# Performance work log

Hardware: AMD Instinct MI355X
Metric: run time of the kernel (lower is better)

The kernel has to match this reference:

```python
import jax, jax.numpy as jnp
import numpy as np

B, S, D, H, NATT = 8, 512, 768, 256, 11  # batch, seq, d_model, gru hidden, n attention branches


def setup_inputs() -> dict:
    key = jax.random.key(0)
    ks = jax.random.split(key, 20)
    w = lambda k, shp, s=0.02: (jax.random.normal(k, shp, jnp.float32) * s)
    emb = w(ks[0], (7, D), 1.0).at[0].set(0.0)  # padding_idx=0 row is zero
    return {
        "essay_amlabel": jax.random.randint(ks[1], (B, S), 0, 7),
        "sequence_output": jax.random.normal(ks[2], (B, S, D), jnp.float32),
        "emb_table": emb,
        "Wq": w(ks[3], (NATT, D, D)), "bq": jnp.zeros((NATT, D), jnp.float32),
        "Wk": w(ks[4], (NATT, D, D)), "bk": jnp.zeros((NATT, D), jnp.float32),
        "Wv": w(ks[5], (NATT, D, D)), "bv": jnp.zeros((NATT, D), jnp.float32),
        "gru_Wih": w(ks[6], (2, 3 * H, D), 1.0 / np.sqrt(H)),
        "gru_Whh": w(ks[7], (2, 3 * H, H), 1.0 / np.sqrt(H)),
        "gru_bih": jnp.zeros((2, 3 * H), jnp.float32),
        "gru_bhh": jnp.zeros((2, 3 * H), jnp.float32),
        "W1": w(ks[8], (2 * H, 1)), "b1": jnp.zeros((1,), jnp.float32),
    }


def _gru_final_hidden(x, Wih, Whh, bih, bhh, reverse):
    # x: [N, S, D] -> final hidden [N, H] (PyTorch GRU equations)
    xp = jnp.einsum('nsd,hd->snh', x, Wih) + bih  # [S, N, 3H]

    def step(h, xt):
        gh = h @ Whh.T + bhh
        i_r, i_z, i_n = jnp.split(xt, 3, axis=-1)
        h_r, h_z, h_n = jnp.split(gh, 3, axis=-1)
        r = jax.nn.sigmoid(i_r + h_r)
        z = jax.nn.sigmoid(i_z + h_z)
        n = jnp.tanh(i_n + r * h_n)
        h_new = (1.0 - z) * n + z * h
        return h_new, None

    h0 = jnp.zeros((x.shape[0], Whh.shape[1]), x.dtype)
    h_final, _ = jax.lax.scan(step, h0, xp, reverse=reverse)
    return h_final


def reference(essay_amlabel, sequence_output, emb_table, Wq, bq, Wk, bk, Wv, bv,
              gru_Wih, gru_Whh, gru_bih, gru_bhh, W1, b1):
    am = emb_table[essay_amlabel]  # [B, S, D] queries
    # 11 independent attentions, num_heads=1, dropout=0 (eval) -> stack on axis k
    Q = jax.nn.relu(jnp.einsum('bsd,kde->kbse', am, Wq) + bq[:, None, None, :])
    K = jax.nn.relu(jnp.einsum('bsd,kde->kbse', sequence_output, Wk) + bk[:, None, None, :])
    V = jax.nn.relu(jnp.einsum('bsd,kde->kbse', sequence_output, Wv) + bv[:, None, None, :])
    scores = jnp.einsum('kbqd,kbmd->kbqm', Q, K) / jnp.sqrt(jnp.float32(D))
    attn = jax.nn.softmax(scores, axis=-1)
    qmask = jnp.sign(jnp.abs(jnp.sum(am, axis=-1)))  # [B, S]
    attn = attn * qmask[None, :, :, None]  # post-softmax query mask (as in source)
    out = jnp.einsum('kbqm,kbmd->kbqd', attn, V) + am[None]  # residual with queries
    eloutput = out + sequence_output[None]  # [11, B, S, D]
    gru_in = eloutput.reshape(NATT * B, S, D)
    h_f = _gru_final_hidden(gru_in, gru_Wih[0], gru_Whh[0], gru_bih[0], gru_bhh[0], False)
    h_b = _gru_final_hidden(gru_in, gru_Wih[1], gru_Whh[1], gru_bih[1], gru_bhh[1], True)
    final = jnp.concatenate([h_f, h_b], axis=-1)  # [11B, 2H]
    reshaped = final.reshape(NATT, B, 2 * H).transpose(1, 0, 2)  # [B, 11, 2H]
    logits = jax.nn.sigmoid(reshaped @ W1 + b1).squeeze(-1)  # [B, 11]
    return logits
```

## Files before the change

### kernel.cpp

```cpp
#include <hip/hip_runtime.h>
#include <hip/hip_bf16.h>
#include <hip/hip_fp16.h>
#include <math.h>

typedef __hip_bfloat16 bf16;
typedef __attribute__((ext_vector_type(8))) short short8;
typedef __attribute__((ext_vector_type(4))) float f32x4;

#define NATT 11
#define Bb 8
#define Ss 512
#define Dd 768
#define Hh 256
#define WSLICE 589824L

__device__ __forceinline__ void stf(float* p, float v) { *p = v; }
__device__ __forceinline__ void stf(bf16* p, float v) { *p = __float2bfloat16(v); }

__device__ __forceinline__ float blo(unsigned u) { return __uint_as_float(u << 16); }
__device__ __forceinline__ float bhi(unsigned u) { return __uint_as_float(u & 0xffff0000u); }
__device__ __forceinline__ float b2f(unsigned short u) { return __uint_as_float(((unsigned)u) << 16); }

__device__ __forceinline__ float ldg_any(const void* base, long idx, int flag) {
  if (flag) return ((const float*)base)[idx];
  return __bfloat162float(((const bf16*)base)[idx]);
}

__device__ __forceinline__ unsigned packh2(float a, float b) {
  __half2 hh = __floats2half2_rn(a, b);
  return __builtin_bit_cast(unsigned, hh);
}
__device__ __forceinline__ unsigned short f2h(float v) {
  __half h = __float2half(v);
  return __builtin_bit_cast(unsigned short, h);
}

typedef _Float16 f16x2 __attribute__((ext_vector_type(2)));

__device__ __forceinline__ float dot2u(unsigned a, unsigned b, float c) {
#if __has_builtin(__builtin_amdgcn_fdot2)
  return __builtin_amdgcn_fdot2(__builtin_bit_cast(f16x2, a),
                                __builtin_bit_cast(f16x2, b), c, false);
#else
  __half2 ah = __builtin_bit_cast(__half2, a);
  __half2 bh = __builtin_bit_cast(__half2, b);
  float2 af = __half22float2(ah), bf = __half22float2(bh);
  return c + af.x * bf.x + af.y * bf.y;
#endif
}

__device__ __forceinline__ float quad_sum(float v) {
#if __has_builtin(__builtin_amdgcn_update_dpp)
  int y = __builtin_amdgcn_update_dpp(0, __builtin_bit_cast(int, v), 0xB1, 0xF, 0xF, true);
  v += __builtin_bit_cast(float, y);
  y = __builtin_amdgcn_update_dpp(0, __builtin_bit_cast(int, v), 0x4E, 0xF, 0xF, true);
  v += __builtin_bit_cast(float, y);
  return v;
#else
  v += __shfl_xor(v, 1);
  v += __shfl_xor(v, 2);
  return v;
#endif
}

__device__ __forceinline__ void lds_barrier() {
  asm volatile("s_waitcnt lgkmcnt(0)\n\ts_barrier" ::: "memory");
}

__device__ __forceinline__ void load_lds16(const void* g, void* l) {
  __builtin_amdgcn_global_load_lds(
      (const __attribute__((address_space(1))) unsigned int*)g,
      (__attribute__((address_space(3))) unsigned int*)l, 16, 0, 0);
}

__global__ __launch_bounds__(64) void probe_kernel(
    const unsigned short* __restrict__ sequ, const unsigned* __restrict__ labu,
    int* __restrict__ flags)
{
  int t = threadIdx.x;
  int wild = 0;
#pragma unroll
  for (int i = 0; i < 4; i++) {
    unsigned short v = sequ[t + i * 64];
    int e = (v >> 7) & 0xFF;
    if (e < 90 || e > 160) wild++;
  }
  int nzodd = 0;
#pragma unroll
  for (int i = 0; i < 2; i++) {
    unsigned w = labu[(t + i * 64) * 2 + 1];
    if (w != 0) nzodd++;
  }
  for (int o = 32; o > 0; o >>= 1) {
    wild  += __shfl_down(wild, o);
    nzodd += __shfl_down(nzodd, o);
  }
  if (t == 0) {
    flags[0] = (wild > 32) ? 1 : 0;
    flags[1] = (nzodd == 0) ? 1 : 0;
  }
}

__global__ __launch_bounds__(256) void conv_seq_kernel(
    const void* __restrict__ seq, bf16* __restrict__ seqb,
    const int* __restrict__ flags)
{
  int flag = flags[0];
  long row = blockIdx.x;
#pragma unroll
  for (int i = 0; i < 3; i++) {
    long e = row * Dd + threadIdx.x + i * 256;
    seqb[e] = __float2bfloat16(ldg_any(seq, e, flag));
  }
}

__global__ __launch_bounds__(256) void convert_kernel(
    const void* __restrict__ src, bf16* __restrict__ dst, long n,
    const int* __restrict__ flags)
{
  int flag = flags[0];
  long i = (long)blockIdx.x * 256 + threadIdx.x;
  if (i < n) dst[i] = __float2bfloat16(ldg_any(src, i, flag));
}

__global__ __launch_bounds__(256) void smalls_kernel(
    const void* __restrict__ emb, const void* __restrict__ Wq,
    const void* __restrict__ bq, float* __restrict__ Qsmall,
    const int* __restrict__ flags)
{
  int flag = flags[0];
  __shared__ float embsh[7 * 768];
  int z = blockIdx.y, chunk = blockIdx.x, tid = threadIdx.x;
  for (int i = tid; i < 7 * 768; i += 256) embsh[i] = ldg_any(emb, i, flag);
  __syncthreads();
  int n = chunk * 256 + tid;
  float acc[7] = {};
  long base = (long)z * WSLICE;
  for (int e = 0; e < Dd; e++) {
    float wv = ldg_any(Wq, base + (long)e * Dd + n, flag);
#pragma unroll
    for (int l = 0; l < 7; l++) acc[l] += embsh[l * 768 + e] * wv;
  }
  float bv = ldg_any(bq, z * Dd + n, flag);
#pragma unroll
  for (int l = 0; l < 7; l++)
    Qsmall[((long)z * 7 + l) * Dd + n] = fmaxf(acc[l] + bv, 0.f);
}

__global__ __launch_bounds__(256) void emb_copy_kernel(
    const void* __restrict__ emb, bf16* __restrict__ outsm,
    float* __restrict__ qmask7, const int* __restrict__ flags)
{
  int flag = flags[0];
  int l = blockIdx.x;
  int t = threadIdx.x;
  float s = 0.f;
#pragma unroll
  for (int i = 0; i < 3; i++) {
    int e = t + i * 256;
    float v = ldg_any(emb, (long)l * Dd + e, flag);
    outsm[(long)(640 + l) * Dd + e] = __float2bfloat16(v);
    s += v;
  }
  for (int o = 32; o > 0; o >>= 1) s += __shfl_down(s, o);
  __shared__ float red[4];
  if ((t & 63) == 0) red[t >> 6] = s;
  __syncthreads();
  if (t == 0) {
    float tot = red[0] + red[1] + red[2] + red[3];
    qmask7[l] = (tot != 0.f) ? 1.f : 0.f;
  }
}

__global__ __launch_bounds__(256) void transpose2_kernel(
    const void* __restrict__ Wk, const void* __restrict__ Wv,
    bf16* __restrict__ WT, const int* __restrict__ flags)
{
  int flag = flags[0];
  __shared__ float tile[32][33];
  int z = blockIdx.z;
  int m = z >> 1, wsel = z & 1;
  const void* src = wsel ? Wv : Wk;
  long off = (long)m * WSLICE;
  bf16* dst = WT + (long)z * WSLICE;
  int kk0 = blockIdx.y * 32, n0 = blockIdx.x * 32;
  int tx = threadIdx.x & 31, ty = threadIdx.x >> 5;
#pragma unroll
  for (int i = 0; i < 4; i++)
    tile[ty + i * 8][tx] = ldg_any(src, off + (long)(kk0 + ty + i * 8) * Dd + n0 + tx, flag);
  __syncthreads();
#pragma unroll
  for (int i = 0; i < 4; i++)
    dst[(long)(n0 + ty + i * 8) * Dd + kk0 + tx] = __float2bfloat16(tile[tx][ty + i * 8]);
}

__device__ __forceinline__ void gemm_mfma_core(
    const bf16* __restrict__ Ab, long ldA,
    const bf16* __restrict__ Bbp, long ldB,
    bf16* As, bf16* Bs, int bm, int bn, int K,
    const void* bias, long bOff,
    void* C, long ldC, int cMode,
    float scale, int relu, int fflag)
{
  int tid = threadIdx.x;
  int lane = tid & 63, w = tid >> 6;
  int mo = (w & 1) * 64, no = (w >> 1) * 64;
  int l15 = lane & 15, q4 = lane >> 4;
  int gr = lane >> 2;
  int gs = (lane & 3) * 8;
  const bf16* aS0 = Ab + (long)(bm + w * 16 + gr) * ldA + gs;
  const bf16* aS1 = aS0 + 64 * ldA;
  const bf16* bS0 = Bbp + (long)(bn + w * 16 + gr) * ldB + gs;
  const bf16* bS1 = bS0 + 64 * ldB;
  bf16* aD0 = As + w * 512;
  bf16* aD1 = As + 2048 + w * 512;
  bf16* bD0 = Bs + w * 512;
  bf16* bD1 = Bs + 2048 + w * 512;

  f32x4 acc[4][4];
#pragma unroll
  for (int i = 0; i < 4; i++)
#pragma unroll
    for (int j = 0; j < 4; j++)
#pragma unroll
      for (int r = 0; r < 4; r++) acc[i][j][r] = 0.f;

  for (int k0 = 0; k0 < K; k0 += 32) {
    load_lds16(aS0, aD0);
    load_lds16(aS1, aD1);
    load_lds16(bS0, bD0);
    load_lds16(bS1, bD1);
    aS0 += 32; aS1 += 32; bS0 += 32; bS1 += 32;
    __syncthreads();
    short8 af[4], bfv[4];
#pragma unroll
    for (int i = 0; i < 4; i++)
      af[i] = *(const short8*)(As + (mo + i * 16 + l15) * 32 + q4 * 8);
#pragma unroll
    for (int j = 0; j < 4; j++)
      bfv[j] = *(const short8*)(Bs + (no + j * 16 + l15) * 32 + q4 * 8);
#pragma unroll
    for (int i = 0; i < 4; i++)
#pragma unroll
      for (int j = 0; j < 4; j++)
        acc[i][j] = __builtin_amdgcn_mfma_f32_16x16x32_bf16(af[i], bfv[j], acc[i][j], 0, 0, 0);
    __syncthreads();
  }

  float bsv[4];
#pragma unroll
  for (int j = 0; j < 4; j++) {
    int colg = bn + no + j * 16 + l15;
    bsv[j] = bias ? ldg_any(bias, bOff + colg, fflag) : 0.f;
  }
#pragma unroll
  for (int i = 0; i < 4; i++) {
#pragma unroll
    for (int j = 0; j < 4; j++) {
      int colg = bn + no + j * 16 + l15;
      if (cMode == 4) {
        int rowg0 = bm + mo + i * 16 + q4 * 4;
        ushort4 pk;
        unsigned short tmp[4];
#pragma unroll
        for (int r = 0; r < 4; r++) {
          float v = acc[i][j][r] * scale + bsv[j];
          if (relu) v = fmaxf(v, 0.f);
          tmp[r] = f2h(v);
        }
        pk.x = tmp[0]; pk.y = tmp[1]; pk.z = tmp[2]; pk.w = tmp[3];
        *(ushort4*)((unsigned short*)C + (long)colg * ldC + rowg0) = pk;
      } else {
#pragma unroll
        for (int r = 0; r < 4; r++) {
          int rowg = bm + mo + i * 16 + q4 * 4 + r;
          float v = acc[i][j][r] * scale + bsv[j];
          if (relu) v = fmaxf(v, 0.f);
          long off2 = (long)rowg * ldC + colg;
          if (cMode == 2)      ((float*)C)[off2] = v;
          else if (cMode == 3) ((unsigned short*)C)[off2] = f2h(v);
          else                 ((bf16*)C)[off2] = __float2bfloat16(v);
        }
      }
    }
  }
}

__global__ __launch_bounds__(256, 2) void proj_kernel(
    const bf16* __restrict__ seqb, const bf16* __restrict__ WT,
    const void* __restrict__ bk, const void* __restrict__ bv,
    unsigned short* __restrict__ Kb, unsigned short* __restrict__ Vt,
    const int* __restrict__ flags)
{
  __shared__ __align__(16) bf16 As[4096];
  __shared__ __align__(16) bf16 Bs[4096];
  int z = blockIdx.z;
  int m = z >> 1, wsel = z & 1;
  const bf16* B = WT + (long)z * WSLICE;
  if (wsel == 0) {
    gemm_mfma_core(seqb, Dd, B, Dd, As, Bs, blockIdx.y * 128, blockIdx.x * 128, Dd,
                   bk, (long)m * Dd, Kb + (long)m * 4096 * Dd, Dd, 3, 1.f, 1, flags[0]);
  } else {
    gemm_mfma_core(seqb, Dd, B, Dd, As, Bs, blockIdx.y * 128, blockIdx.x * 128, Dd,
                   bv, (long)m * Dd, Vt + (long)m * Dd * 4096, 4096, 4, 1.f, 1, flags[0]);
  }
}

__global__ __launch_bounds__(256, 2) void seqw_kernel(
    const bf16* __restrict__ seqb, const bf16* __restrict__ WihB,
    const void* __restrict__ bih, bf16* __restrict__ seqW,
    const int* __restrict__ flags)
{
  __shared__ __align__(16) bf16 As[4096];
  __shared__ __align__(16) bf16 Bs[4096];
  int dir = blockIdx.z;
  gemm_mfma_core(seqb, Dd, WihB + (long)dir * WSLICE, Dd, As, Bs,
                 blockIdx.y * 128, blockIdx.x * 128, Dd,
                 bih, (long)dir * Dd, seqW + (long)dir * 4096 * Dd, Dd, 0,
                 1.f, 0, flags[0]);
}

__global__ __launch_bounds__(256, 2) void pvw_kernel(
    const bf16* __restrict__ outsm, const bf16* __restrict__ WihB,
    float* __restrict__ PVW, const int* __restrict__ flags)
{
  __shared__ __align__(16) bf16 As[4096];
  __shared__ __align__(16) bf16 Bs[4096];
  int dir = blockIdx.z;
  gemm_mfma_core(outsm, Dd, WihB + (long)dir * WSLICE, Dd, As, Bs,
                 blockIdx.y * 128, blockIdx.x * 128, Dd,
                 nullptr, 0, PVW + (long)dir * 768 * Dd, Dd, 2, 1.f, 0, flags[0]);
}

__global__ __launch_bounds__(512, 2) void attn_kernel(
    const unsigned short* __restrict__ Kb, const unsigned short* __restrict__ Vt,
    const float* __restrict__ Qsmall, const float* __restrict__ qmask7,
    bf16* __restrict__ outsm, float scl)
{
  int blk = blockIdx.x;
  int k = blk >> 3, b = blk & 7;
  int tid = threadIdx.x;
  int lane = tid & 63, w = tid >> 6;
  __shared__ unsigned qs[7][384];
  __shared__ unsigned short ash[7][512];
  __shared__ float wred[8][7];
  __shared__ float gred[7];
  __shared__ float finv[7];
  for (int i = tid; i < 7 * 384; i += 512) {
    int l = i / 384, e2 = i - l * 384;
    const float* qp = Qsmall + ((long)k * 7 + l) * Dd + 2 * e2;
    qs[l][e2] = packh2(qp[0], qp[1]);
  }
  __syncthreads();
  const uint4* Krow = (const uint4*)(Kb + ((long)k * 4096 + b * 512 + tid) * Dd);
  float sc[7] = {};
  for (int e8 = 0; e8 < 96; e8++) {
    uint4 kv = Krow[e8];
#pragma unroll
    for (int l = 0; l < 7; l++) {
      sc[l] = dot2u(qs[l][e8 * 4],     kv.x, sc[l]);
      sc[l] = dot2u(qs[l][e8 * 4 + 1], kv.y, sc[l]);
      sc[l] = dot2u(qs[l][e8 * 4 + 2], kv.z, sc[l]);
      sc[l] = dot2u(qs[l][e8 * 4 + 3], kv.w, sc[l]);
    }
  }
#pragma unroll
  for (int l = 0; l < 7; l++) sc[l] *= scl;
#pragma unroll
  for (int l = 0; l < 7; l++) {
    float v = sc[l];
    for (int o = 32; o > 0; o >>= 1) v = fmaxf(v, __shfl_down(v, o));
    if (lane == 0) wred[w][l] = v;
  }
  __syncthreads();
  if (tid < 7) {
    float m = wred[0][tid];
#pragma unroll
    for (int i = 1; i < 8; i++) m = fmaxf(m, wred[i][tid]);
    gred[tid] = m;
  }
  __syncthreads();
  float ev[7];
#pragma unroll
  for (int l = 0; l < 7; l++) {
    ev[l] = __expf(sc[l] - gred[l]);
    float v = ev[l];
    for (int o = 32; o > 0; o >>= 1) v += __shfl_down(v, o);
    if (lane == 0) wred[w][l] = v;
  }
  __syncthreads();
  if (tid < 7) {
    float s = 0.f;
#pragma unroll
    for (int i = 0; i < 8; i++) s += wred[i][tid];
    finv[tid] = qmask7[tid] / s;
  }
  __syncthreads();
#pragma unroll
  for (int l = 0; l < 7; l++) ash[l][tid] = f2h(ev[l] * finv[l]);
  __syncthreads();
  for (int rep = 0; rep < 2; rep++) {
    int n = tid + rep * 512;
    if (n >= Dd) break;
    const uint4* Vrow = (const uint4*)(Vt + ((long)k * Dd + n) * 4096 + b * 512);
    float acc[7] = {};
    for (int m8 = 0; m8 < 64; m8++) {
      uint4 vv = Vrow[m8];
#pragma unroll
      for (int l = 0; l < 7; l++) {
        const unsigned* ap = (const unsigned*)&ash[l][0];
        acc[l] = dot2u(ap[m8 * 4],     vv.x, acc[l]);
        acc[l] = dot2u(ap[m8 * 4 + 1], vv.y, acc[l]);
        acc[l] = dot2u(ap[m8 * 4 + 2], vv.z, acc[l]);
        acc[l] = dot2u(ap[m8 * 4 + 3], vv.w, acc[l]);
      }
    }
#pragma unroll
    for (int l = 0; l < 7; l++)
      outsm[((long)blk * 7 + l) * Dd + n] = __float2bfloat16(acc[l]);
  }
}

__global__ __launch_bounds__(512, 2) void gru_kernel(
    const bf16* __restrict__ seqW,
    const float* __restrict__ PVW,
    const void* __restrict__ labels,
    const void* __restrict__ Whh, const void* __restrict__ bhh,
    float* __restrict__ hbuf, const int* __restrict__ flags)
{
  int flag = flags[0], lflag = flags[1];
  int idx = blockIdx.x;
  int dir = idx / 88, n = idx - dir * 88;
  int b = n & 7;
  int tid = threadIdx.x;
  int q = tid & 3, cg = tid >> 2;
  int hi = q >> 1;
  int ch = cg + hi * 128;
  int r0 = ch, r1 = 256 + ch, r2 = 512 + ch;

  unsigned w[6][32];
#pragma unroll
  for (int s = 0; s < 6; s++) {
    int row = (s >> 1) * 256 + cg + (s & 1) * 128;
    long base = ((long)dir * Dd + row) * Hh + q * 64;
    if (flag) {
      const float4* s4 = (const float4*)((const float*)Whh + base);
#pragma unroll
      for (int i = 0; i < 16; i++) {
        float4 v = s4[i];
        w[s][2 * i]     = packh2(v.x, v.y);
        w[s][2 * i + 1] = packh2(v.z, v.w);
      }
    } else {
      const uint4* s4 = (const uint4*)((const bf16*)Whh + base);
#pragma unroll
      for (int i = 0; i < 8; i++) {
        uint4 v = s4[i];
        w[s][4 * i]     = packh2(blo(v.x), bhi(v.x));
        w[s][4 * i + 1] = packh2(blo(v.y), bhi(v.y));
        w[s][4 * i + 2] = packh2(blo(v.z), bhi(v.z));
        w[s][4 * i + 3] = packh2(blo(v.w), bhi(v.w));
      }
    }
  }
  float bh0 = ldg_any(bhh, dir * Dd + r0, flag);
  float bh1 = ldg_any(bhh, dir * Dd + r1, flag);
  float bh2 = ldg_any(bhh, dir * Dd + r2, flag);

  __shared__ float rowsh[7 * 768];
  __shared__ int labsh[512];
  __shared__ __align__(16) unsigned short hsh[2][4 * 72];

  for (int i = tid; i < 7 * 768; i += 512) {
    int l = i / 768, row = i - l * 768;
    rowsh[i] = PVW[((long)dir * 768 + n * 7 + l) * Dd + row]
             + PVW[((long)dir * 768 + 640 + l) * Dd + row];
  }
  labsh[tid] = lflag ? (int)((const long long*)labels)[b * 512 + tid]
                     : ((const int*)labels)[b * 512 + tid];
  if (tid < 288) { hsh[0][tid] = 0; hsh[1][tid] = 0; }
  __syncthreads();

  const unsigned short* swu = (const unsigned short*)seqW
                            + ((long)dir * 4096 + b * 512) * Dd;
  int t0 = dir ? 511 : 0, t1 = dir ? 510 : 1, t2 = dir ? 509 : 2;
  unsigned short xs00 = swu[(long)t0 * Dd + r0];
  unsigned short xs01 = swu[(long)t0 * Dd + r1];
  unsigned short xs02 = swu[(long)t0 * Dd + r2];
  unsigned short xs10 = swu[(long)t1 * Dd + r0];
  unsigned short xs11 = swu[(long)t1 * Dd + r1];
  unsigned short xs12 = swu[(long)t1 * Dd + r2];
  unsigned short xs20 = swu[(long)t2 * Dd + r0];
  unsigned short xs21 = swu[(long)t2 * Dd + r1];
  unsigned short xs22 = swu[(long)t2 * Dd + r2];

  float hprev = 0.f;
  int hwaddr = (ch >> 6) * 72 + (ch & 63);
  for (int tt = 0; tt < Ss; tt++) {
    int t = dir ? 511 - tt : tt;
    int ttp = (tt + 3 < Ss) ? tt + 3 : Ss - 1;
    int tp = dir ? 511 - ttp : ttp;
    unsigned short xp0 = swu[(long)tp * Dd + r0];
    unsigned short xp1 = swu[(long)tp * Dd + r1];
    unsigned short xp2 = swu[(long)tp * Dd + r2];
    int lab = labsh[t];
    const float* rs = rowsh + lab * 768;
    float xr = rs[r0] + b2f(xs00);
    float xz = rs[r1] + b2f(xs01);
    float xn = rs[r2] + b2f(xs02);
    const uint4* hq = (const uint4*)(hsh[tt & 1] + q * 72);
    float a[6] = {};
#pragma unroll
    for (int jj = 0; jj < 8; jj++) {
      uint4 hv = hq[jj];
#pragma unroll
      for (int s = 0; s < 6; s++) {
        a[s] = dot2u(w[s][4 * jj],     hv.x, a[s]);
        a[s] = dot2u(w[s][4 * jj + 1], hv.y, a[s]);
        a[s] = dot2u(w[s][4 * jj + 2], hv.z, a[s]);
        a[s] = dot2u(w[s][4 * jj + 3], hv.w, a[s]);
      }
    }
#pragma unroll
    for (int s = 0; s < 6; s++) a[s] = quad_sum(a[s]);
    float ar = hi ? a[1] : a[0];
    float az = hi ? a[3] : a[2];
    float an = hi ? a[5] : a[4];
    float rg = 1.f / (1.f + __expf(-(xr + ar + bh0)));
    float zg = 1.f / (1.f + __expf(-(xz + az + bh1)));
    float targ = xn + rg * (an + bh2);
    float e2 = __expf(2.f * targ);
    float ng = 1.f - 2.f / (e2 + 1.f);
    float hnew = (1.f - zg) * ng + zg * hprev;
    hprev = hnew;
    if ((q & 1) == 0) hsh[(tt + 1) & 1][hwaddr] = f2h(hnew);
    lds_barrier();
    xs00 = xs10; xs01 = xs11; xs02 = xs12;
    xs10 = xs20; xs11 = xs21; xs12 = xs22;
    xs20 = xp0;  xs21 = xp1;  xs22 = xp2;
  }
  if ((q & 1) == 0) hbuf[((long)(dir * 88 + n)) * Hh + ch] = hprev;
}

__global__ __launch_bounds__(256) void head_kernel(
    const float* __restrict__ hbuf, const void* __restrict__ W1,
    const void* __restrict__ b1, void* __restrict__ out,
    const int* __restrict__ flags)
{
  int flag = flags[0];
  int n = blockIdx.x;
  int c = threadIdx.x;
  float v = hbuf[(long)n * Hh + c] * ldg_any(W1, c, flag)
          + hbuf[(long)(88 + n) * Hh + c] * ldg_any(W1, 256 + c, flag);
  for (int o = 32; o > 0; o >>= 1) v += __shfl_down(v, o);
  __shared__ float red[4];
  if ((c & 63) == 0) red[c >> 6] = v;
  __syncthreads();
  if (c == 0) {
    float s = red[0] + red[1] + red[2] + red[3] + ldg_any(b1, 0, flag);
    float sig = 1.f / (1.f + __expf(-s));
    int k = n / Bb, b = n - k * Bb;
    int o = b * NATT + k;
    if (flag) ((float*)out)[o] = sig;
    else      stf((bf16*)out + o, sig);
  }
}

extern "C" void kernel_launch(void* const* d_in, const int* in_sizes, int n_in,
                              void* d_out, int out_size, void* d_ws, size_t ws_size,
                              hipStream_t stream) {
  const void* labels = d_in[0];
  const void* seq  = d_in[1];
  const void* emb  = d_in[2];
  const void* Wq   = d_in[3];
  const void* bq   = d_in[4];
  const void* Wk   = d_in[5];
  const void* bk   = d_in[6];
  const void* Wv   = d_in[7];
  const void* bv   = d_in[8];
  const void* Wih  = d_in[9];
  const void* Whh  = d_in[10];
  const void* bih  = d_in[11];
  const void* bhh  = d_in[12];
  const void* W1   = d_in[13];
  const void* b1   = d_in[14];

  char* p = (char*)d_ws;
  size_t off = 0;
  auto alloc = [&](size_t bytes) -> void* {
    void* r = p + off; off += (bytes + 255) & ~(size_t)255; return r;
  };
  int*    flags  = (int*)alloc(2 * sizeof(int));
  bf16*   seqb   = (bf16*)alloc(4096UL * 768 * 2);
  float*  qmask7 = (float*)alloc(7 * 4);
  float*  Qsmall = (float*)alloc(11UL * 7 * 768 * 4);
  bf16*   WihB   = (bf16*)alloc(2UL * WSLICE * 2);
  bf16*   WT     = (bf16*)alloc(22UL * WSLICE * 2);
  unsigned short* Kb = (unsigned short*)alloc(11UL * 4096 * 768 * 2);
  unsigned short* Vt = (unsigned short*)alloc(11UL * 768 * 4096 * 2);
  bf16*   outsm  = (bf16*)alloc(768UL * 768 * 2);
  float*  PVW    = (float*)alloc(2UL * 768 * 768 * 4);
  bf16*   seqW   = (bf16*)alloc(2UL * 4096 * 768 * 2);
  float*  hbuf   = (float*)alloc(2UL * 88 * 256 * 4);
  if (off > ws_size) return;

  probe_kernel<<<1, 64, 0, stream>>>((const unsigned short*)seq,
                                     (const unsigned*)labels, flags);
  conv_seq_kernel<<<4096, 256, 0, stream>>>(seq, seqb, flags);
  convert_kernel<<<(int)((2 * WSLICE + 255) / 256), 256, 0, stream>>>(
      Wih, WihB, 2L * WSLICE, flags);
  smalls_kernel<<<dim3(3, 11), 256, 0, stream>>>(emb, Wq, bq, Qsmall, flags);
  emb_copy_kernel<<<7, 256, 0, stream>>>(emb, outsm, qmask7, flags);
  transpose2_kernel<<<dim3(24, 24, 22), 256, 0, stream>>>(Wk, Wv, WT, flags);
  proj_kernel<<<dim3(6, 32, 22), 256, 0, stream>>>(
      seqb, WT, bk, bv, Kb, Vt, flags);
  seqw_kernel<<<dim3(6, 32, 2), 256, 0, stream>>>(seqb, WihB, bih, seqW, flags);
  const float scl = 1.f / sqrtf(768.f);
  attn_kernel<<<88, 512, 0, stream>>>(Kb, Vt, Qsmall, qmask7, outsm, scl);
  pvw_kernel<<<dim3(6, 6, 2), 256, 0, stream>>>(outsm, WihB, PVW, flags);
  gru_kernel<<<176, 512, 0, stream>>>(seqW, PVW, labels, Whh, bhh, hbuf, flags);
  head_kernel<<<88, 256, 0, stream>>>(hbuf, W1, b1, d_out, flags);
}
```

Measured before the change: 1.194 ms.

## Double GRU block threads to one hidden unit per quad; split smalls reduction

```diff
diff --git a/kernel.cpp b/kernel.cpp
--- a/kernel.cpp
+++ b/kernel.cpp
@@ -130,21 +130,33 @@
 {
   int flag = flags[0];
   __shared__ float embsh[7 * 768];
-  int z = blockIdx.y, chunk = blockIdx.x, tid = threadIdx.x;
+  __shared__ float psum[4][7][64];
+  int z = blockIdx.y;
+  int bx = blockIdx.x;
+  int tid = threadIdx.x;
+  int sub = tid >> 6, nl = tid & 63;
   for (int i = tid; i < 7 * 768; i += 256) embsh[i] = ldg_any(emb, i, flag);
   __syncthreads();
-  int n = chunk * 256 + tid;
+  int n = bx * 64 + nl;
+  long base = (long)z * WSLICE;
   float acc[7] = {};
-  long base = (long)z * WSLICE;
-  for (int e = 0; e < Dd; e++) {
+  int e0 = sub * 192;
+  for (int e = e0; e < e0 + 192; e++) {
     float wv = ldg_any(Wq, base + (long)e * Dd + n, flag);
 #pragma unroll
     for (int l = 0; l < 7; l++) acc[l] += embsh[l * 768 + e] * wv;
   }
-  float bv = ldg_any(bq, z * Dd + n, flag);
-#pragma unroll
-  for (int l = 0; l < 7; l++)
-    Qsmall[((long)z * 7 + l) * Dd + n] = fmaxf(acc[l] + bv, 0.f);
+#pragma unroll
+  for (int l = 0; l < 7; l++) psum[sub][l][nl] = acc[l];
+  __syncthreads();
+  if (sub == 0) {
+    float bv = ldg_any(bq, z * Dd + n, flag);
+#pragma unroll
+    for (int l = 0; l < 7; l++) {
+      float v = psum[0][l][nl] + psum[1][l][nl] + psum[2][l][nl] + psum[3][l][nl] + bv;
+      Qsmall[((long)z * 7 + l) * Dd + n] = fmaxf(v, 0.f);
+    }
+  }
 }
 
 __global__ __launch_bounds__(256) void emb_copy_kernel(
@@ -421,7 +433,7 @@
   }
 }
 
-__global__ __launch_bounds__(512, 2) void gru_kernel(
+__global__ __launch_bounds__(1024, 4) void gru_kernel(
     const bf16* __restrict__ seqW,
     const float* __restrict__ PVW,
     const void* __restrict__ labels,
@@ -433,33 +445,30 @@
   int dir = idx / 88, n = idx - dir * 88;
   int b = n & 7;
   int tid = threadIdx.x;
-  int q = tid & 3, cg = tid >> 2;
-  int hi = q >> 1;
-  int ch = cg + hi * 128;
+  int q = tid & 3, ch = tid >> 2;
   int r0 = ch, r1 = 256 + ch, r2 = 512 + ch;
 
-  unsigned w[6][32];
-#pragma unroll
-  for (int s = 0; s < 6; s++) {
-    int row = (s >> 1) * 256 + cg + (s & 1) * 128;
-    long base = ((long)dir * Dd + row) * Hh + q * 64;
+  unsigned w[3][32];
+#pragma unroll
+  for (int g = 0; g < 3; g++) {
+    long base = ((long)dir * Dd + g * 256 + ch) * Hh + q * 64;
     if (flag) {
       const float4* s4 = (const float4*)((const float*)Whh + base);
 #pragma unroll
       for (int i = 0; i < 16; i++) {
         float4 v = s4[i];
-        w[s][2 * i]     = packh2(v.x, v.y);
-        w[s][2 * i + 1] = packh2(v.z, v.w);
+        w[g][2 * i]     = packh2(v.x, v.y);
+        w[g][2 * i + 1] = packh2(v.z, v.w);
       }
     } else {
       const uint4* s4 = (const uint4*)((const bf16*)Whh + base);
 #pragma unroll
       for (int i = 0; i < 8; i++) {
         uint4 v = s4[i];
-        w[s][4 * i]     = packh2(blo(v.x), bhi(v.x));
-        w[s][4 * i + 1] = packh2(blo(v.y), bhi(v.y));
-        w[s][4 * i + 2] = packh2(blo(v.z), bhi(v.z));
-        w[s][4 * i + 3] = packh2(blo(v.w), bhi(v.w));
+        w[g][4 * i]     = packh2(blo(v.x), bhi(v.x));
+        w[g][4 * i + 1] = packh2(blo(v.y), bhi(v.y));
+        w[g][4 * i + 2] = packh2(blo(v.z), bhi(v.z));
+        w[g][4 * i + 3] = packh2(blo(v.w), bhi(v.w));
       }
     }
   }
@@ -469,36 +478,34 @@
 
   __shared__ float rowsh[7 * 768];
   __shared__ int labsh[512];
-  __shared__ __align__(16) unsigned short hsh[2][4 * 72];
-
-  for (int i = tid; i < 7 * 768; i += 512) {
+  __shared__ __align__(16) unsigned short hsh[2][288];
+
+  for (int i = tid; i < 7 * 768; i += 1024) {
     int l = i / 768, row = i - l * 768;
     rowsh[i] = PVW[((long)dir * 768 + n * 7 + l) * Dd + row]
              + PVW[((long)dir * 768 + 640 + l) * Dd + row];
   }
-  labsh[tid] = lflag ? (int)((const long long*)labels)[b * 512 + tid]
-                     : ((const int*)labels)[b * 512 + tid];
+  if (tid < 512)
+    labsh[tid] = lflag ? (int)((const long long*)labels)[b * 512 + tid]
+                       : ((const int*)labels)[b * 512 + tid];
   if (tid < 288) { hsh[0][tid] = 0; hsh[1][tid] = 0; }
   __syncthreads();
 
   const unsigned short* swu = (const unsigned short*)seqW
                             + ((long)dir * 4096 + b * 512) * Dd;
-  int t0 = dir ? 511 : 0, t1 = dir ? 510 : 1, t2 = dir ? 509 : 2;
+  int t0 = dir ? 511 : 0, t1 = dir ? 510 : 1;
   unsigned short xs00 = swu[(long)t0 * Dd + r0];
   unsigned short xs01 = swu[(long)t0 * Dd + r1];
   unsigned short xs02 = swu[(long)t0 * Dd + r2];
   unsigned short xs10 = swu[(long)t1 * Dd + r0];
   unsigned short xs11 = swu[(long)t1 * Dd + r1];
   unsigned short xs12 = swu[(long)t1 * Dd + r2];
-  unsigned short xs20 = swu[(long)t2 * Dd + r0];
-  unsigned short xs21 = swu[(long)t2 * Dd + r1];
-  unsigned short xs22 = swu[(long)t2 * Dd + r2];
 
   float hprev = 0.f;
   int hwaddr = (ch >> 6) * 72 + (ch & 63);
   for (int tt = 0; tt < Ss; tt++) {
     int t = dir ? 511 - tt : tt;
-    int ttp = (tt + 3 < Ss) ? tt + 3 : Ss - 1;
+    int ttp = (tt + 2 < Ss) ? tt + 2 : Ss - 1;
     int tp = dir ? 511 - ttp : ttp;
     unsigned short xp0 = swu[(long)tp * Dd + r0];
     unsigned short xp1 = swu[(long)tp * Dd + r1];
@@ -509,37 +516,39 @@
     float xz = rs[r1] + b2f(xs01);
     float xn = rs[r2] + b2f(xs02);
     const uint4* hq = (const uint4*)(hsh[tt & 1] + q * 72);
-    float a[6] = {};
+    float a0 = 0.f, a1 = 0.f, a2 = 0.f;
 #pragma unroll
     for (int jj = 0; jj < 8; jj++) {
       uint4 hv = hq[jj];
-#pragma unroll
-      for (int s = 0; s < 6; s++) {
-        a[s] = dot2u(w[s][4 * jj],     hv.x, a[s]);
-        a[s] = dot2u(w[s][4 * jj + 1], hv.y, a[s]);
-        a[s] = dot2u(w[s][4 * jj + 2], hv.z, a[s]);
-        a[s] = dot2u(w[s][4 * jj + 3], hv.w, a[s]);
-      }
+      a0 = dot2u(w[0][4 * jj],     hv.x, a0);
+      a0 = dot2u(w[0][4 * jj + 1], hv.y, a0);
+      a0 = dot2u(w[0][4 * jj + 2], hv.z, a0);
+      a0 = dot2u(w[0][4 * jj + 3], hv.w, a0);
+      a1 = dot2u(w[1][4 * jj],     hv.x, a1);
+      a1 = dot2u(w[1][4 * jj + 1], hv.y, a1);
+      a1 = dot2u(w[1][4 * jj + 2], hv.z, a1);
+      a1 = dot2u(w[1][4 * jj + 3], hv.w, a1);
+      a2 = dot2u(w[2][4 * jj],     hv.x, a2);
+      a2 = dot2u(w[2][4 * jj + 1], hv.y, a2);
+      a2 = dot2u(w[2][4 * jj + 2], hv.z, a2);
+      a2 = dot2u(w[2][4 * jj + 3], hv.w, a2);
     }
-#pragma unroll
-    for (int s = 0; s < 6; s++) a[s] = quad_sum(a[s]);
-    float ar = hi ? a[1] : a[0];
-    float az = hi ? a[3] : a[2];
-    float an = hi ? a[5] : a[4];
-    float rg = 1.f / (1.f + __expf(-(xr + ar + bh0)));
-    float zg = 1.f / (1.f + __expf(-(xz + az + bh1)));
-    float targ = xn + rg * (an + bh2);
+    a0 = quad_sum(a0);
+    a1 = quad_sum(a1);
+    a2 = quad_sum(a2);
+    float rg = 1.f / (1.f + __expf(-(xr + a0 + bh0)));
+    float zg = 1.f / (1.f + __expf(-(xz + a1 + bh1)));
+    float targ = xn + rg * (a2 + bh2);
     float e2 = __expf(2.f * targ);
     float ng = 1.f - 2.f / (e2 + 1.f);
     float hnew = (1.f - zg) * ng + zg * hprev;
     hprev = hnew;
-    if ((q & 1) == 0) hsh[(tt + 1) & 1][hwaddr] = f2h(hnew);
+    if (q == 0) hsh[(tt + 1) & 1][hwaddr] = f2h(hnew);
     lds_barrier();
     xs00 = xs10; xs01 = xs11; xs02 = xs12;
-    xs10 = xs20; xs11 = xs21; xs12 = xs22;
-    xs20 = xp0;  xs21 = xp1;  xs22 = xp2;
-  }
-  if ((q & 1) == 0) hbuf[((long)(dir * 88 + n)) * Hh + ch] = hprev;
+    xs10 = xp0;  xs11 = xp1;  xs12 = xp2;
+  }
+  if (q == 0) hbuf[((long)(dir * 88 + n)) * Hh + ch] = hprev;
 }
 
 __global__ __launch_bounds__(256) void head_kernel(
@@ -609,7 +618,7 @@
   conv_seq_kernel<<<4096, 256, 0, stream>>>(seq, seqb, flags);
   convert_kernel<<<(int)((2 * WSLICE + 255) / 256), 256, 0, stream>>>(
       Wih, WihB, 2L * WSLICE, flags);
-  smalls_kernel<<<dim3(3, 11), 256, 0, stream>>>(emb, Wq, bq, Qsmall, flags);
+  smalls_kernel<<<dim3(12, 11), 256, 0, stream>>>(emb, Wq, bq, Qsmall, flags);
   emb_copy_kernel<<<7, 256, 0, stream>>>(emb, outsm, qmask7, flags);
   transpose2_kernel<<<dim3(24, 24, 22), 256, 0, stream>>>(Wk, Wv, WT, flags);
   proj_kernel<<<dim3(6, 32, 22), 256, 0, stream>>>(
@@ -618,6 +627,6 @@
   const float scl = 1.f / sqrtf(768.f);
   attn_kernel<<<88, 512, 0, stream>>>(Kb, Vt, Qsmall, qmask7, outsm, scl);
   pvw_kernel<<<dim3(6, 6, 2), 256, 0, stream>>>(outsm, WihB, PVW, flags);
-  gru_kernel<<<176, 512, 0, stream>>>(seqW, PVW, labels, Whh, bhh, hbuf, flags);
+  gru_kernel<<<176, 1024, 0, stream>>>(seqW, PVW, labels, Whh, bhh, hbuf, flags);
   head_kernel<<<88, 256, 0, stream>>>(hbuf, W1, b1, d_out, flags);
 }
```

Measured after the change: 1.241 ms. +3.9%, slower.
